# Optimization experiments

Measured on AMD Instinct MI355X. Metric: run time of the kernel, lower is better.

Reference implementation:

```python
import jax, jax.numpy as jnp
import numpy as np

EDGE_DROPOUT = 0.1   # init kwarg edge_dropout
TRAINING = True      # init kwarg is_training
N_NODES = 8192
D_FEAT = 512


def setup_inputs() -> dict:
    key = jax.random.key(0)
    x = jax.random.normal(key, (N_NODES, D_FEAT), dtype=jnp.float32)
    return {"x": x, "k": 30}


def _graph_process(x, k):
    # knn_fast: cosine similarity kNN with symmetric degree normalization.
    n = x.shape[0]
    xn = x / jnp.linalg.norm(x, axis=1, keepdims=True)      # F.normalize(x, dim=1)
    sim = xn @ xn.T                                         # [n, n] (torch does this in blocks of 1000; same math)
    vals, inds = jax.lax.top_k(sim, k + 1)                  # [n, k+1]
    rows = jnp.broadcast_to(jnp.arange(n)[:, None], vals.shape).reshape(-1)
    cols = inds.reshape(-1)
    v = vals.reshape(-1)
    norm_row = vals.sum(axis=1)                             # out-degree mass
    norm_col = jnp.zeros(n, vals.dtype).at[cols].add(v)     # in-degree mass (index_add_)
    norm = norm_row + norm_col
    v = v * (norm[rows] ** -0.5) * (norm[cols] ** -0.5)
    # values[torch.isnan(values)] = 0
    v = jnp.where(jnp.isnan(v), jnp.zeros_like(v), v)
    # symmetrize edge list
    rows_ = jnp.concatenate([rows, cols])
    cols_ = jnp.concatenate([cols, rows])
    v_ = jnp.concatenate([v, v])
    v_ = jax.nn.relu(v_)
    if TRAINING and EDGE_DROPOUT > 0.0:
        keep = jax.random.bernoulli(jax.random.key(42), 1.0 - EDGE_DROPOUT, v_.shape)
        v_ = jnp.where(keep, v_ / (1.0 - EDGE_DROPOUT), jnp.zeros_like(v_))
    # sparse_coo_tensor(...).coalesce(): duplicate (i,j) entries sum -> dense scatter-add
    adj = jnp.zeros((n, n), v_.dtype).at[rows_, cols_].add(v_)
    return adj


def reference(x, k):
    return _graph_process(x, k)
```

## Files before the change

kernel.cpp:

```cpp
#include <hip/hip_runtime.h>
#include <cstdint>
#include <cmath>

#define NN 8192
#define DD 512
#define KP1 31
#define HALF_EDGES (NN * KP1)

typedef float f2 __attribute__((ext_vector_type(2)));

__device__ __forceinline__ uint32_t rotl32(uint32_t v, int s) {
  return (v << s) | (v >> (32 - s));
}

__device__ __forceinline__ void threefry2x32_42(uint32_t x0, uint32_t x1,
                                                uint32_t& o0, uint32_t& o1) {
  const uint32_t ks0 = 0u, ks1 = 42u;
  const uint32_t ks2 = 0x1BD11BDAu ^ ks0 ^ ks1;
  x0 += ks0; x1 += ks1;
  x0 += x1; x1 = rotl32(x1, 13); x1 ^= x0;
  x0 += x1; x1 = rotl32(x1, 15); x1 ^= x0;
  x0 += x1; x1 = rotl32(x1, 26); x1 ^= x0;
  x0 += x1; x1 = rotl32(x1, 6);  x1 ^= x0;
  x0 += ks1; x1 += ks2 + 1u;
  x0 += x1; x1 = rotl32(x1, 17); x1 ^= x0;
  x0 += x1; x1 = rotl32(x1, 29); x1 ^= x0;
  x0 += x1; x1 = rotl32(x1, 16); x1 ^= x0;
  x0 += x1; x1 = rotl32(x1, 24); x1 ^= x0;
  x0 += ks2; x1 += ks0 + 2u;
  x0 += x1; x1 = rotl32(x1, 13); x1 ^= x0;
  x0 += x1; x1 = rotl32(x1, 15); x1 ^= x0;
  x0 += x1; x1 = rotl32(x1, 26); x1 ^= x0;
  x0 += x1; x1 = rotl32(x1, 6);  x1 ^= x0;
  x0 += ks0; x1 += ks1 + 3u;
  x0 += x1; x1 = rotl32(x1, 17); x1 ^= x0;
  x0 += x1; x1 = rotl32(x1, 29); x1 ^= x0;
  x0 += x1; x1 = rotl32(x1, 16); x1 ^= x0;
  x0 += x1; x1 = rotl32(x1, 24); x1 ^= x0;
  x0 += ks1; x1 += ks2 + 4u;
  x0 += x1; x1 = rotl32(x1, 13); x1 ^= x0;
  x0 += x1; x1 = rotl32(x1, 15); x1 ^= x0;
  x0 += x1; x1 = rotl32(x1, 26); x1 ^= x0;
  x0 += x1; x1 = rotl32(x1, 6);  x1 ^= x0;
  x0 += ks2; x1 += ks0 + 5u;
  o0 = x0; o1 = x1;
}

__device__ __forceinline__ bool keep_edge(uint32_t e) {
  uint32_t y0, y1;
  threefry2x32_42(0u, e, y0, y1);
  uint32_t bits = y0 ^ y1;
  float u = __uint_as_float((bits >> 9) | 0x3f800000u) - 1.0f;
  return u < 0.9f;
}

__global__ __launch_bounds__(256) void rownorm_kernel(const float* __restrict__ x,
                                                      float* __restrict__ nrm) {
#pragma clang fp contract(off)
  __shared__ float rowbuf[16][DD];
  __shared__ float partial[16][4];
  int tid = threadIdx.x;
  int rowbase = blockIdx.x * 16;

  for (int p = 0; p < 8; ++p) {
    int f = tid + p * 256;
    int r = f >> 7, k4 = f & 127;
    *(float4*)(&rowbuf[r][k4 << 2]) =
        *(const float4*)(x + (size_t)(rowbase + r) * DD + (k4 << 2));
  }
  __syncthreads();
  if (tid < 64) {
    int r = tid >> 2, q = tid & 3;
    const float* s = &rowbuf[r][q * 128];
    float a0 = s[0]*s[0], a1 = s[1]*s[1], a2 = s[2]*s[2], a3 = s[3]*s[3];
    float a4 = s[4]*s[4], a5 = s[5]*s[5], a6 = s[6]*s[6], a7 = s[7]*s[7];
    for (int i = 8; i < 128; i += 8) {
      a0 += s[i+0]*s[i+0]; a1 += s[i+1]*s[i+1];
      a2 += s[i+2]*s[i+2]; a3 += s[i+3]*s[i+3];
      a4 += s[i+4]*s[i+4]; a5 += s[i+5]*s[i+5];
      a6 += s[i+6]*s[i+6]; a7 += s[i+7]*s[i+7];
    }
    partial[r][q] = ((a0 + a1) + (a2 + a3)) + ((a4 + a5) + (a6 + a7));
  }
  __syncthreads();
  if (tid < 16) {
    float S = (partial[tid][0] + partial[tid][1]) + (partial[tid][2] + partial[tid][3]);
    nrm[rowbase + tid] = sqrtf(S);
  }
}

__global__ __launch_bounds__(256) void xnorm_kernel(const float* __restrict__ x,
                                                    const float* __restrict__ nrm,
                                                    float* __restrict__ xn) {
#pragma clang fp contract(off)
  int idx = blockIdx.x * 256 + threadIdx.x;
  const float4* xv = (const float4*)x;
  float4* xo = (float4*)xn;
  float4 v = xv[idx];
  float n = nrm[idx >> 7];
  v.x = v.x / n; v.y = v.y / n; v.z = v.z / n; v.w = v.w / n;
  xo[idx] = v;
}

template <bool PRE>
__global__ __launch_bounds__(256, 2) void gemm_kernel(const float* __restrict__ x,
                                                      const float* __restrict__ nrm,
                                                      float* __restrict__ out) {
#pragma clang fp contract(off)
  int bid = blockIdx.x;
  int by = (int)((129.0f - sqrtf(16641.0f - 8.0f * (float)bid)) * 0.5f);
  while (64 * by - (by * (by - 1)) / 2 > bid) --by;
  while (64 * (by + 1) - ((by + 1) * by) / 2 <= bid) ++by;
  const int bx = by + (bid - (64 * by - (by * (by - 1)) / 2));

  extern __shared__ char smem[];
  float4* AsF4 = (float4*)smem;
  float*  Bs   = (float*)(smem + 16384);

  const int tid = threadIdx.x;
  const int rb = by * 128;
  const int cb = bx * 128;
  const int m = tid & 7;
  const int g = tid >> 3;

  float nA[4], nB[4];
  if (!PRE) {
    #pragma unroll
    for (int p = 0; p < 4; ++p) {
      nA[p] = nrm[rb + g + 32 * p];
      nB[p] = nrm[cb + g + 32 * p];
    }
  }

  const int lane = tid & 63, wave = tid >> 6;
  const int wr = wave >> 1, wc = wave & 1;
  const int lr = lane >> 3, lc = lane & 7;
  const int r0 = wr * 64 + lr * 8;
  const int c0 = wc * 64 + lc * 8;

  f2 acc[8][4];
  #pragma unroll
  for (int i = 0; i < 8; ++i)
    #pragma unroll
    for (int jp = 0; jp < 4; ++jp) { acc[i][jp].x = 0.f; acc[i][jp].y = 0.f; }

  const float4* xv = (const float4*)x;

  float4 ra[4], rbv[4];
  #pragma unroll
  for (int p = 0; p < 4; ++p) {
    int r = g + 32 * p;
    ra[p]  = xv[(size_t)(rb + r) * 128 + m];
    rbv[p] = xv[(size_t)(cb + r) * 128 + m];
  }

  for (int kc = 0; kc < 16; ++kc) {
    __syncthreads();
    #pragma unroll
    for (int p = 0; p < 4; ++p) {
      int r = g + 32 * p;
      float4 va = ra[p];
      if (!PRE) {
        va.x = va.x / nA[p]; va.y = va.y / nA[p];
        va.z = va.z / nA[p]; va.w = va.w / nA[p];
      }
      AsF4[r * 8 + ((m + (r >> 3)) & 7)] = va;
      float4 vb = rbv[p];
      if (!PRE) {
        vb.x = vb.x / nB[p]; vb.y = vb.y / nB[p];
        vb.z = vb.z / nB[p]; vb.w = vb.w / nB[p];
      }
      float* bp = Bs + (4 * m) * 128 + (r ^ ((m & 3) << 3));
      bp[0]   = vb.x;
      bp[128] = vb.y;
      bp[256] = vb.z;
      bp[384] = vb.w;
    }
    __syncthreads();
    if (kc < 15) {
      #pragma unroll
      for (int p = 0; p < 4; ++p) {
        int r = g + 32 * p;
        ra[p]  = xv[(size_t)(rb + r) * 128 + (kc + 1) * 8 + m];
        rbv[p] = xv[(size_t)(cb + r) * 128 + (kc + 1) * 8 + m];
      }
    }

    #pragma unroll 2
    for (int k4 = 0; k4 < 8; ++k4) {
      float4 av[8];
      const int tA = (k4 + (r0 >> 3)) & 7;
      #pragma unroll
      for (int i = 0; i < 8; ++i) av[i] = AsF4[(r0 + i) * 8 + tA];
      float4 b01[8];
      const int csw = c0 ^ ((k4 & 3) << 3);
      #pragma unroll
      for (int kk = 0; kk < 4; ++kk) {
        const float* bp = Bs + (4 * k4 + kk) * 128 + csw;
        b01[2 * kk]     = *(const float4*)(bp);
        b01[2 * kk + 1] = *(const float4*)(bp + 4);
      }
      #pragma unroll
      for (int kk = 0; kk < 4; ++kk) {
        f2 bb0 = {b01[2 * kk].x,     b01[2 * kk].y};
        f2 bb1 = {b01[2 * kk].z,     b01[2 * kk].w};
        f2 bb2 = {b01[2 * kk + 1].x, b01[2 * kk + 1].y};
        f2 bb3 = {b01[2 * kk + 1].z, b01[2 * kk + 1].w};
        #pragma unroll
        for (int i = 0; i < 8; ++i) {
          float a = ((const float*)&av[i])[kk];
          f2 t0 = a * bb0; acc[i][0] = acc[i][0] + t0;
          f2 t1 = a * bb1; acc[i][1] = acc[i][1] + t1;
          f2 t2 = a * bb2; acc[i][2] = acc[i][2] + t2;
          f2 t3 = a * bb3; acc[i][3] = acc[i][3] + t3;
        }
      }
    }
  }

  float4* outv = (float4*)out;

  #pragma unroll
  for (int i = 0; i < 8; ++i) {
    #pragma unroll
    for (int h = 0; h < 2; ++h) {
      float4 o;
      o.x = acc[i][2 * h].x;     o.y = acc[i][2 * h].y;
      o.z = acc[i][2 * h + 1].x; o.w = acc[i][2 * h + 1].y;
      outv[(size_t)(rb + r0 + i) * 2048 + ((cb + c0) >> 2) + h] = o;
    }
  }

  if (rb != cb) {
    float* Cs = (float*)smem;
    #pragma unroll 1
    for (int q = 0; q < 4; ++q) {
      __syncthreads();
      if (wr == (q >> 1) && (lr >> 2) == (q & 1)) {
        const int rB = (lr & 3) * 8;
        #pragma unroll
        for (int i = 0; i < 8; ++i) {
          #pragma unroll
          for (int jp = 0; jp < 4; ++jp)
            *(f2*)(Cs + (rB + i) * 130 + wc * 64 + lc * 8 + 2 * jp) = acc[i][jp];
        }
      }
      __syncthreads();
      #pragma unroll
      for (int q2 = 0; q2 < 4; ++q2) {
        int f = tid + q2 * 256;
        int c = f >> 3, t4 = f & 7;
        float4 o;
        o.x = Cs[(4 * t4 + 0) * 130 + c];
        o.y = Cs[(4 * t4 + 1) * 130 + c];
        o.z = Cs[(4 * t4 + 2) * 130 + c];
        o.w = Cs[(4 * t4 + 3) * 130 + c];
        outv[(size_t)(cb + c) * 2048 + ((rb + q * 32) >> 2) + t4] = o;
      }
    }
  }
}

__global__ __launch_bounds__(256) void topk_kernel(const float* __restrict__ sim,
                                                   float* __restrict__ vals,
                                                   int* __restrict__ inds) {
  const int w = threadIdx.x >> 6;
  const int lane = threadIdx.x & 63;
  const int row = blockIdx.x * 4 + w;

  float kval = -1e30f;
  int   kidx = 0;
  float kmin = -1e30f;

  const float* srow = sim + (size_t)row * NN;
  for (int grp = 0; grp < NN / 64; ++grp) {
    float v = srow[grp * 64 + lane];
    unsigned long long mask = __ballot(v > kmin);
    while (mask) {
      int src = __builtin_ctzll(mask);
      mask &= mask - 1;
      float vv = __shfl(v, src, 64);
      if (vv > kmin) {
        int cc = grp * 64 + src;
        unsigned long long ge = __ballot(kval >= vv) & 0x7FFFFFFFull;
        int pos = __popcll(ge);
        float upv = __shfl_up(kval, 1, 64);
        int   upi = __shfl_up(kidx, 1, 64);
        if (lane < KP1) {
          if (lane == pos) { kval = vv; kidx = cc; }
          else if (lane > pos) { kval = upv; kidx = upi; }
        }
        kmin = __shfl(kval, KP1 - 1, 64);
      }
    }
  }
  if (lane < KP1) {
    vals[(size_t)row * KP1 + lane] = kval;
    inds[row * KP1 + lane] = kidx;
  }
}

__global__ __launch_bounds__(256) void norm_kernel(const float* __restrict__ vals,
                                                   const int* __restrict__ inds,
                                                   float* __restrict__ norm) {
  int i = blockIdx.x * blockDim.x + threadIdx.x;
  if (i >= NN) return;
  float s = 0.f;
  for (int t = 0; t < KP1; ++t) {
    float v = vals[i * KP1 + t];
    s += v;
    atomicAdd(&norm[inds[i * KP1 + t]], v);
  }
  atomicAdd(&norm[i], s);
}

__global__ __launch_bounds__(256) void scatter_kernel(const float* __restrict__ vals,
                                                      const int* __restrict__ inds,
                                                      const float* __restrict__ norm,
                                                      float* __restrict__ out) {
  int e = blockIdx.x * blockDim.x + threadIdx.x;
  if (e >= HALF_EDGES) return;
  int i = e / KP1;
  int c = inds[e];
  float v = vals[e];
  float nv = v * (1.0f / sqrtf(norm[i])) * (1.0f / sqrtf(norm[c]));
  if (isnan(nv)) nv = 0.f;
  nv = fmaxf(nv, 0.f);
  float scaled = nv / 0.9f;
  if (keep_edge((uint32_t)e))
    atomicAdd(out + (size_t)i * NN + c, scaled);
  if (keep_edge((uint32_t)(e + HALF_EDGES)))
    atomicAdd(out + (size_t)c * NN + i, scaled);
}

extern "C" void kernel_launch(void* const* d_in, const int* in_sizes, int n_in,
                              void* d_out, int out_size, void* d_ws, size_t ws_size,
                              hipStream_t stream) {
  (void)in_sizes; (void)n_in;
  const float* x = (const float*)d_in[0];
  float* out = (float*)d_out;

  float* nrm  = (float*)d_ws;
  float* vals = nrm + NN;
  int*   inds = (int*)(vals + HALF_EDGES);
  float* norm = (float*)(inds + HALF_EDGES);
  float* xn   = (float*)((char*)d_ws + (size_t)(2 * 1024 * 1024));
  const bool pre = ws_size >= (size_t)(2 * 1024 * 1024) + (size_t)NN * DD * 4;

  hipLaunchKernelGGL(rownorm_kernel, dim3(NN / 16), dim3(256), 0, stream, x, nrm);
  if (pre) {
    hipLaunchKernelGGL(xnorm_kernel, dim3(NN * DD / 4 / 256), dim3(256), 0, stream,
                       x, nrm, xn);
    hipLaunchKernelGGL((gemm_kernel<true>), dim3(2080), dim3(256), 32768, stream,
                       xn, (const float*)nullptr, out);
  } else {
    hipLaunchKernelGGL((gemm_kernel<false>), dim3(2080), dim3(256), 32768, stream,
                       x, nrm, out);
  }
  hipLaunchKernelGGL(topk_kernel, dim3(NN / 4), dim3(256), 0, stream,
                     out, vals, inds);
  hipMemsetAsync(norm, 0, NN * sizeof(float), stream);
  hipLaunchKernelGGL(norm_kernel, dim3((NN + 255) / 256), dim3(256), 0, stream,
                     vals, inds, norm);
  hipMemsetAsync(d_out, 0, (size_t)out_size * sizeof(float), stream);
  hipLaunchKernelGGL(scatter_kernel, dim3((HALF_EDGES + 255) / 256), dim3(256), 0, stream,
                     vals, inds, norm, out);
}
```

Measured before the change: 1.103 ms.

## Double-buffer GEMM tiles and stage A via direct global-to-LDS loads

Replaces the templated GEMM with a dedicated pre-normalized kernel that uses K-chunks of 16 with double-buffered shared memory. The A tile is loaded with global_load_lds, which writes straight into LDS without passing through registers, while the B tile is prefetched two stages ahead through registers. This needs one barrier per iteration instead of two, overlapping loads with FMA work and cutting register pressure. The fallback path keeps the old design under a new name. The risks are more loop iterations and correctness of the swizzle and async-load ordering.

Measured after the change: 1.111 ms. Within noise of the previous version (+0.8%).

```diff
diff --git a/kernel.cpp b/kernel.cpp
--- a/kernel.cpp
+++ b/kernel.cpp
@@ -54,6 +54,12 @@
   return u < 0.9f;
 }
 
+__device__ __forceinline__ void gll16(const float4* gsrc, void* lds) {
+  __builtin_amdgcn_global_load_lds(
+      (const __attribute__((address_space(1))) uint32_t*)gsrc,
+      (__attribute__((address_space(3))) uint32_t*)lds, 16, 0, 0);
+}
+
 __global__ __launch_bounds__(256) void rownorm_kernel(const float* __restrict__ x,
                                                       float* __restrict__ nrm) {
 #pragma clang fp contract(off)
@@ -102,10 +108,8 @@
   xo[idx] = v;
 }
 
-template <bool PRE>
-__global__ __launch_bounds__(256, 2) void gemm_kernel(const float* __restrict__ x,
-                                                      const float* __restrict__ nrm,
-                                                      float* __restrict__ out) {
+__global__ __launch_bounds__(256, 2) void gemm_kernel_pre(const float* __restrict__ x,
+                                                          float* __restrict__ out) {
 #pragma clang fp contract(off)
   int bid = blockIdx.x;
   int by = (int)((129.0f - sqrtf(16641.0f - 8.0f * (float)bid)) * 0.5f);
@@ -113,6 +117,164 @@
   while (64 * (by + 1) - ((by + 1) * by) / 2 <= bid) ++by;
   const int bx = by + (bid - (64 * by - (by * (by - 1)) / 2));
 
+  __shared__ __align__(16) char smem[32768];
+  float4* AsF4 = (float4*)smem;
+  float*  Bs   = (float*)(smem + 16384);
+
+  const int tid = threadIdx.x;
+  const int rb = by * 128;
+  const int cb = bx * 128;
+  const int m = tid & 3;
+  const int g = tid >> 2;
+
+  const int lane = tid & 63, wave = tid >> 6;
+  const int wr = wave >> 1, wc = wave & 1;
+  const int lr = lane >> 3, lc = lane & 7;
+  const int r0 = wr * 64 + lr * 8;
+  const int c0 = wc * 64 + lc * 8;
+  const int r3 = r0 >> 3;
+
+  f2 acc[8][4];
+  #pragma unroll
+  for (int i = 0; i < 8; ++i)
+    #pragma unroll
+    for (int jp = 0; jp < 4; ++jp) { acc[i][jp].x = 0.f; acc[i][jp].y = 0.f; }
+
+  const float4* xv = (const float4*)x;
+  float4 rbv[2];
+
+  int gr[2], gs[2];
+  #pragma unroll
+  for (int q = 0; q < 2; ++q) {
+    int fi = wave * 128 + q * 64 + lane;
+    gr[q] = fi >> 2;
+    gs[q] = ((fi & 3) - (gr[q] >> 3)) & 3;
+  }
+
+  auto stage_A = [&](int nbuf, int t) {
+    #pragma unroll
+    for (int q = 0; q < 2; ++q)
+      gll16(xv + (size_t)(rb + gr[q]) * 128 + t * 4 + gs[q],
+            (void*)(AsF4 + nbuf * 512 + wave * 128 + q * 64));
+  };
+  auto load_B = [&](int t) {
+    #pragma unroll
+    for (int p = 0; p < 2; ++p)
+      rbv[p] = xv[(size_t)(cb + g + 64 * p) * 128 + t * 4 + m];
+  };
+  auto write_B = [&](int nbuf) {
+    #pragma unroll
+    for (int p = 0; p < 2; ++p) {
+      int r = g + 64 * p;
+      float* bp = Bs + nbuf * 2048 + (4 * m) * 128 + (r ^ (m << 3));
+      bp[0]   = rbv[p].x;
+      bp[128] = rbv[p].y;
+      bp[256] = rbv[p].z;
+      bp[384] = rbv[p].w;
+    }
+  };
+
+  load_B(0);
+  write_B(0);
+  stage_A(0, 0);
+  load_B(1);
+
+  #pragma unroll 1
+  for (int t = 0; t < 32; ++t) {
+    const int buf = t & 1;
+    __syncthreads();
+    if (t < 31) {
+      stage_A(buf ^ 1, t + 1);
+      write_B(buf ^ 1);
+      if (t < 30) load_B(t + 2);
+    }
+    const float4* Ab = AsF4 + buf * 512;
+    const float*  Bb = Bs + buf * 2048;
+    #pragma unroll
+    for (int k4 = 0; k4 < 4; ++k4) {
+      float4 av[8];
+      const int tA = (k4 + r3) & 3;
+      #pragma unroll
+      for (int i = 0; i < 8; ++i) av[i] = Ab[(r0 + i) * 4 + tA];
+      const int csw = c0 ^ (k4 << 3);
+      #pragma unroll
+      for (int kk = 0; kk < 4; ++kk) {
+        const float* bp = Bb + (4 * k4 + kk) * 128 + csw;
+        float4 b0 = *(const float4*)(bp);
+        float4 b1 = *(const float4*)(bp + 4);
+        f2 bb0 = {b0.x, b0.y};
+        f2 bb1 = {b0.z, b0.w};
+        f2 bb2 = {b1.x, b1.y};
+        f2 bb3 = {b1.z, b1.w};
+        #pragma unroll
+        for (int i = 0; i < 8; ++i) {
+          float a = ((const float*)&av[i])[kk];
+          f2 t0 = a * bb0;
+          f2 t1 = a * bb1;
+          f2 t2 = a * bb2;
+          f2 t3 = a * bb3;
+          acc[i][0] = acc[i][0] + t0;
+          acc[i][1] = acc[i][1] + t1;
+          acc[i][2] = acc[i][2] + t2;
+          acc[i][3] = acc[i][3] + t3;
+        }
+      }
+    }
+  }
+
+  float4* outv = (float4*)out;
+
+  #pragma unroll
+  for (int i = 0; i < 8; ++i) {
+    #pragma unroll
+    for (int h = 0; h < 2; ++h) {
+      float4 o;
+      o.x = acc[i][2 * h].x;     o.y = acc[i][2 * h].y;
+      o.z = acc[i][2 * h + 1].x; o.w = acc[i][2 * h + 1].y;
+      outv[(size_t)(rb + r0 + i) * 2048 + ((cb + c0) >> 2) + h] = o;
+    }
+  }
+
+  if (rb != cb) {
+    float* Cs = (float*)smem;
+    #pragma unroll 1
+    for (int q = 0; q < 4; ++q) {
+      __syncthreads();
+      if (wr == (q >> 1) && (lr >> 2) == (q & 1)) {
+        const int rB = (lr & 3) * 8;
+        #pragma unroll
+        for (int i = 0; i < 8; ++i) {
+          #pragma unroll
+          for (int jp = 0; jp < 4; ++jp)
+            *(f2*)(Cs + (rB + i) * 130 + wc * 64 + lc * 8 + 2 * jp) = acc[i][jp];
+        }
+      }
+      __syncthreads();
+      #pragma unroll
+      for (int q2 = 0; q2 < 4; ++q2) {
+        int f = tid + q2 * 256;
+        int c = f >> 3, t4 = f & 7;
+        float4 o;
+        o.x = Cs[(4 * t4 + 0) * 130 + c];
+        o.y = Cs[(4 * t4 + 1) * 130 + c];
+        o.z = Cs[(4 * t4 + 2) * 130 + c];
+        o.w = Cs[(4 * t4 + 3) * 130 + c];
+        outv[(size_t)(cb + c) * 2048 + ((rb + q * 32) >> 2) + t4] = o;
+      }
+    }
+  }
+}
+
+__global__ __launch_bounds__(256, 2) void gemm_kernel_fb(const float* __restrict__ x,
+                                                         const float* __restrict__ nrm,
+                                                         float* __restrict__ out) {
+#pragma clang fp contract(off)
+  int bid = blockIdx.x;
+  int by = (int)((129.0f - sqrtf(16641.0f - 8.0f * (float)bid)) * 0.5f);
+  while (64 * by - (by * (by - 1)) / 2 > bid) --by;
+  while (64 * (by + 1) - ((by + 1) * by) / 2 <= bid) ++by;
+  const int bx = by + (bid - (64 * by - (by * (by - 1)) / 2));
+
   extern __shared__ char smem[];
   float4* AsF4 = (float4*)smem;
   float*  Bs   = (float*)(smem + 16384);
@@ -124,12 +286,10 @@
   const int g = tid >> 3;
 
   float nA[4], nB[4];
-  if (!PRE) {
-    #pragma unroll
-    for (int p = 0; p < 4; ++p) {
-      nA[p] = nrm[rb + g + 32 * p];
-      nB[p] = nrm[cb + g + 32 * p];
-    }
+  #pragma unroll
+  for (int p = 0; p < 4; ++p) {
+    nA[p] = nrm[rb + g + 32 * p];
+    nB[p] = nrm[cb + g + 32 * p];
   }
 
   const int lane = tid & 63, wave = tid >> 6;
@@ -137,6 +297,7 @@
   const int lr = lane >> 3, lc = lane & 7;
   const int r0 = wr * 64 + lr * 8;
   const int c0 = wc * 64 + lc * 8;
+  const int r3 = r0 >> 3;
 
   f2 acc[8][4];
   #pragma unroll
@@ -145,7 +306,6 @@
     for (int jp = 0; jp < 4; ++jp) { acc[i][jp].x = 0.f; acc[i][jp].y = 0.f; }
 
   const float4* xv = (const float4*)x;
-
   float4 ra[4], rbv[4];
   #pragma unroll
   for (int p = 0; p < 4; ++p) {
@@ -160,17 +320,13 @@
     for (int p = 0; p < 4; ++p) {
       int r = g + 32 * p;
       float4 va = ra[p];
-      if (!PRE) {
-        va.x = va.x / nA[p]; va.y = va.y / nA[p];
-        va.z = va.z / nA[p]; va.w = va.w / nA[p];
-      }
+      va.x = va.x / nA[p]; va.y = va.y / nA[p];
+      va.z = va.z / nA[p]; va.w = va.w / nA[p];
       AsF4[r * 8 + ((m + (r >> 3)) & 7)] = va;
       float4 vb = rbv[p];
-      if (!PRE) {
-        vb.x = vb.x / nB[p]; vb.y = vb.y / nB[p];
-        vb.z = vb.z / nB[p]; vb.w = vb.w / nB[p];
-      }
-      float* bp = Bs + (4 * m) * 128 + (r ^ ((m & 3) << 3));
+      vb.x = vb.x / nB[p]; vb.y = vb.y / nB[p];
+      vb.z = vb.z / nB[p]; vb.w = vb.w / nB[p];
+      float* bp = Bs + (4 * m) * 128 + (r ^ (m << 3));
       bp[0]   = vb.x;
       bp[128] = vb.y;
       bp[256] = vb.z;
@@ -189,11 +345,11 @@
     #pragma unroll 2
     for (int k4 = 0; k4 < 8; ++k4) {
       float4 av[8];
-      const int tA = (k4 + (r0 >> 3)) & 7;
+      const int tA = (k4 + r3) & 7;
       #pragma unroll
       for (int i = 0; i < 8; ++i) av[i] = AsF4[(r0 + i) * 8 + tA];
       float4 b01[8];
-      const int csw = c0 ^ ((k4 & 3) << 3);
+      const int csw = c0 ^ (k4 << 3);
       #pragma unroll
       for (int kk = 0; kk < 4; ++kk) {
         const float* bp = Bs + (4 * k4 + kk) * 128 + csw;
@@ -209,17 +365,20 @@
         #pragma unroll
         for (int i = 0; i < 8; ++i) {
           float a = ((const float*)&av[i])[kk];
-          f2 t0 = a * bb0; acc[i][0] = acc[i][0] + t0;
-          f2 t1 = a * bb1; acc[i][1] = acc[i][1] + t1;
-          f2 t2 = a * bb2; acc[i][2] = acc[i][2] + t2;
-          f2 t3 = a * bb3; acc[i][3] = acc[i][3] + t3;
+          f2 t0 = a * bb0;
+          f2 t1 = a * bb1;
+          f2 t2 = a * bb2;
+          f2 t3 = a * bb3;
+          acc[i][0] = acc[i][0] + t0;
+          acc[i][1] = acc[i][1] + t1;
+          acc[i][2] = acc[i][2] + t2;
+          acc[i][3] = acc[i][3] + t3;
         }
       }
     }
   }
 
   float4* outv = (float4*)out;
-
   #pragma unroll
   for (int i = 0; i < 8; ++i) {
     #pragma unroll
@@ -230,7 +389,6 @@
       outv[(size_t)(rb + r0 + i) * 2048 + ((cb + c0) >> 2) + h] = o;
     }
   }
-
   if (rb != cb) {
     float* Cs = (float*)smem;
     #pragma unroll 1
@@ -351,10 +509,10 @@
   if (pre) {
     hipLaunchKernelGGL(xnorm_kernel, dim3(NN * DD / 4 / 256), dim3(256), 0, stream,
                        x, nrm, xn);
-    hipLaunchKernelGGL((gemm_kernel<true>), dim3(2080), dim3(256), 32768, stream,
-                       xn, (const float*)nullptr, out);
+    hipLaunchKernelGGL(gemm_kernel_pre, dim3(2080), dim3(256), 0, stream,
+                       xn, out);
   } else {
-    hipLaunchKernelGGL((gemm_kernel<false>), dim3(2080), dim3(256), 32768, stream,
+    hipLaunchKernelGGL(gemm_kernel_fb, dim3(2080), dim3(256), 32768, stream,
                        x, nrm, out);
   }
   hipLaunchKernelGGL(topk_kernel, dim3(NN / 4), dim3(256), 0, stream,
```

## Fuse norm with transpose and use 1024-thread async-LDS GEMM with swizzled tile order

Applied to the files above, without the earlier changes.

Merges the row-norm and normalize kernels into one kernel that also writes the normalized matrix transposed (k-major), so the GEMM can stage contiguous tiles straight into LDS with global_load_lds in a double-buffered loop. The new GEMM runs 1024 threads per block with a 4x4 register tile, remaps block ids to interleave triangle tiles, and writes the mirrored tile directly with transposed stores instead of going through LDS. It drops one pass over x and the register-staged loads. In exchange each thread keeps a much smaller register tile, which lowers arithmetic intensity per LDS read, and the transposed writes of the mirror tile are strided. The fallback GEMM also gets a tweaked B-swizzle.

Result: slower. 1.150 ms (+4.3%).

```diff
diff --git a/kernel.cpp b/kernel.cpp
--- a/kernel.cpp
+++ b/kernel.cpp
@@ -54,6 +54,12 @@
   return u < 0.9f;
 }
 
+__device__ __forceinline__ void gll16(const float4* gsrc, void* lds) {
+  __builtin_amdgcn_global_load_lds(
+      (const __attribute__((address_space(1))) uint32_t*)gsrc,
+      (__attribute__((address_space(3))) uint32_t*)lds, 16, 0, 0);
+}
+
 __global__ __launch_bounds__(256) void rownorm_kernel(const float* __restrict__ x,
                                                       float* __restrict__ nrm) {
 #pragma clang fp contract(off)
@@ -89,23 +95,154 @@
   }
 }
 
-__global__ __launch_bounds__(256) void xnorm_kernel(const float* __restrict__ x,
-                                                    const float* __restrict__ nrm,
-                                                    float* __restrict__ xn) {
+__global__ __launch_bounds__(256) void normT_kernel(const float* __restrict__ x,
+                                                    float* __restrict__ nrm,
+                                                    float* __restrict__ xnt) {
 #pragma clang fp contract(off)
-  int idx = blockIdx.x * 256 + threadIdx.x;
-  const float4* xv = (const float4*)x;
-  float4* xo = (float4*)xn;
-  float4 v = xv[idx];
-  float n = nrm[idx >> 7];
-  v.x = v.x / n; v.y = v.y / n; v.z = v.z / n; v.w = v.w / n;
-  xo[idx] = v;
-}
-
-template <bool PRE>
-__global__ __launch_bounds__(256, 2) void gemm_kernel(const float* __restrict__ x,
-                                                      const float* __restrict__ nrm,
-                                                      float* __restrict__ out) {
+  __shared__ float rowbuf[16][DD];
+  __shared__ float partial[16][4];
+  __shared__ float snrm[16];
+  int tid = threadIdx.x;
+  int rowbase = blockIdx.x * 16;
+
+  for (int p = 0; p < 8; ++p) {
+    int f = tid + p * 256;
+    int r = f >> 7, k4 = f & 127;
+    *(float4*)(&rowbuf[r][k4 << 2]) =
+        *(const float4*)(x + (size_t)(rowbase + r) * DD + (k4 << 2));
+  }
+  __syncthreads();
+  if (tid < 64) {
+    int r = tid >> 2, q = tid & 3;
+    const float* s = &rowbuf[r][q * 128];
+    float a0 = s[0]*s[0], a1 = s[1]*s[1], a2 = s[2]*s[2], a3 = s[3]*s[3];
+    float a4 = s[4]*s[4], a5 = s[5]*s[5], a6 = s[6]*s[6], a7 = s[7]*s[7];
+    for (int i = 8; i < 128; i += 8) {
+      a0 += s[i+0]*s[i+0]; a1 += s[i+1]*s[i+1];
+      a2 += s[i+2]*s[i+2]; a3 += s[i+3]*s[i+3];
+      a4 += s[i+4]*s[i+4]; a5 += s[i+5]*s[i+5];
+      a6 += s[i+6]*s[i+6]; a7 += s[i+7]*s[i+7];
+    }
+    partial[r][q] = ((a0 + a1) + (a2 + a3)) + ((a4 + a5) + (a6 + a7));
+  }
+  __syncthreads();
+  if (tid < 16) {
+    float S = (partial[tid][0] + partial[tid][1]) + (partial[tid][2] + partial[tid][3]);
+    float n = sqrtf(S);
+    nrm[rowbase + tid] = n;
+    snrm[tid] = n;
+  }
+  __syncthreads();
+  for (int kq = 0; kq < 2; ++kq) {
+    int k = tid * 2 + kq;
+    #pragma unroll
+    for (int rq = 0; rq < 4; ++rq) {
+      float4 o;
+      o.x = rowbuf[rq * 4 + 0][k] / snrm[rq * 4 + 0];
+      o.y = rowbuf[rq * 4 + 1][k] / snrm[rq * 4 + 1];
+      o.z = rowbuf[rq * 4 + 2][k] / snrm[rq * 4 + 2];
+      o.w = rowbuf[rq * 4 + 3][k] / snrm[rq * 4 + 3];
+      *(float4*)(xnt + (size_t)k * NN + rowbase + rq * 4) = o;
+    }
+  }
+}
+
+__global__ __launch_bounds__(1024) void gemm_kernel_pre2(const float* __restrict__ xnt,
+                                                         float* __restrict__ out) {
+#pragma clang fp contract(off)
+  int bid0 = blockIdx.x;
+  int bid = (bid0 & 7) * 260 + (bid0 >> 3);
+  int by = (int)((129.0f - sqrtf(16641.0f - 8.0f * (float)bid)) * 0.5f);
+  while (64 * by - (by * (by - 1)) / 2 > bid) --by;
+  while (64 * (by + 1) - ((by + 1) * by) / 2 <= bid) ++by;
+  const int bx = by + (bid - (64 * by - (by * (by - 1)) / 2));
+
+  __shared__ __align__(16) char smem[32768];
+  float* As = (float*)smem;
+  float* Bs = (float*)(smem + 16384);
+
+  const int tid  = threadIdx.x;
+  const int lane = tid & 63, wave = tid >> 6;
+  const int rb = by * 128, cb = bx * 128;
+
+  const int wr = wave >> 2, wc = wave & 3;
+  const int lr = lane >> 3, lc = lane & 7;
+  const int r0 = wr * 32 + lr * 4;
+  const int c0 = wc * 32 + lc * 4;
+
+  f2 acc[4][2];
+  #pragma unroll
+  for (int i = 0; i < 4; ++i) {
+    acc[i][0].x = 0.f; acc[i][0].y = 0.f;
+    acc[i][1].x = 0.f; acc[i][1].y = 0.f;
+  }
+
+  const bool stA = wave < 8;
+  const int w8 = stA ? wave : wave - 8;
+  const int kl = w8 * 2 + (lane >> 5);
+  const size_t gcol = (size_t)(stA ? rb : cb) + (lane & 31) * 4;
+  float* ldst = (stA ? As : Bs) + w8 * 256;
+
+  auto stage = [&](int nbuf, int t) {
+    gll16((const float4*)(xnt + (size_t)(t * 16 + kl) * NN + gcol),
+          (void*)(ldst + nbuf * 2048));
+  };
+
+  stage(0, 0);
+
+  #pragma unroll 1
+  for (int t = 0; t < 32; ++t) {
+    const int buf = t & 1;
+    __syncthreads();
+    if (t < 31) stage(buf ^ 1, t + 1);
+    const float* Ab = As + buf * 2048 + r0;
+    const float* Bb = Bs + buf * 2048 + c0;
+    #pragma unroll
+    for (int k = 0; k < 16; ++k) {
+      float4 a = *(const float4*)(Ab + k * 128);
+      float4 b = *(const float4*)(Bb + k * 128);
+      f2 bb0 = {b.x, b.y};
+      f2 bb1 = {b.z, b.w};
+      #pragma unroll
+      for (int i = 0; i < 4; ++i) {
+        float av = ((const float*)&a)[i];
+        f2 t0 = av * bb0;
+        f2 t1 = av * bb1;
+        acc[i][0] = acc[i][0] + t0;
+        acc[i][1] = acc[i][1] + t1;
+      }
+    }
+  }
+
+  float4* outv = (float4*)out;
+
+  #pragma unroll
+  for (int i = 0; i < 4; ++i) {
+    float4 o;
+    o.x = acc[i][0].x; o.y = acc[i][0].y;
+    o.z = acc[i][1].x; o.w = acc[i][1].y;
+    outv[(size_t)(rb + r0 + i) * 2048 + ((cb + c0) >> 2)] = o;
+  }
+  if (rb != cb) {
+    #pragma unroll
+    for (int j = 0; j < 4; ++j) {
+      const int jh = j >> 1;
+      float4 o;
+      if (j & 1) {
+        o.x = acc[0][jh].y; o.y = acc[1][jh].y;
+        o.z = acc[2][jh].y; o.w = acc[3][jh].y;
+      } else {
+        o.x = acc[0][jh].x; o.y = acc[1][jh].x;
+        o.z = acc[2][jh].x; o.w = acc[3][jh].x;
+      }
+      outv[(size_t)(cb + c0 + j) * 2048 + ((rb + r0) >> 2)] = o;
+    }
+  }
+}
+
+__global__ __launch_bounds__(256, 2) void gemm_kernel_fb(const float* __restrict__ x,
+                                                         const float* __restrict__ nrm,
+                                                         float* __restrict__ out) {
 #pragma clang fp contract(off)
   int bid = blockIdx.x;
   int by = (int)((129.0f - sqrtf(16641.0f - 8.0f * (float)bid)) * 0.5f);
@@ -124,12 +261,10 @@
   const int g = tid >> 3;
 
   float nA[4], nB[4];
-  if (!PRE) {
-    #pragma unroll
-    for (int p = 0; p < 4; ++p) {
-      nA[p] = nrm[rb + g + 32 * p];
-      nB[p] = nrm[cb + g + 32 * p];
-    }
+  #pragma unroll
+  for (int p = 0; p < 4; ++p) {
+    nA[p] = nrm[rb + g + 32 * p];
+    nB[p] = nrm[cb + g + 32 * p];
   }
 
   const int lane = tid & 63, wave = tid >> 6;
@@ -137,6 +272,7 @@
   const int lr = lane >> 3, lc = lane & 7;
   const int r0 = wr * 64 + lr * 8;
   const int c0 = wc * 64 + lc * 8;
+  const int r3 = r0 >> 3;
 
   f2 acc[8][4];
   #pragma unroll
@@ -145,7 +281,6 @@
     for (int jp = 0; jp < 4; ++jp) { acc[i][jp].x = 0.f; acc[i][jp].y = 0.f; }
 
   const float4* xv = (const float4*)x;
-
   float4 ra[4], rbv[4];
   #pragma unroll
   for (int p = 0; p < 4; ++p) {
@@ -160,17 +295,13 @@
     for (int p = 0; p < 4; ++p) {
       int r = g + 32 * p;
       float4 va = ra[p];
-      if (!PRE) {
-        va.x = va.x / nA[p]; va.y = va.y / nA[p];
-        va.z = va.z / nA[p]; va.w = va.w / nA[p];
-      }
+      va.x = va.x / nA[p]; va.y = va.y / nA[p];
+      va.z = va.z / nA[p]; va.w = va.w / nA[p];
       AsF4[r * 8 + ((m + (r >> 3)) & 7)] = va;
       float4 vb = rbv[p];
-      if (!PRE) {
-        vb.x = vb.x / nB[p]; vb.y = vb.y / nB[p];
-        vb.z = vb.z / nB[p]; vb.w = vb.w / nB[p];
-      }
-      float* bp = Bs + (4 * m) * 128 + (r ^ ((m & 3) << 3));
+      vb.x = vb.x / nB[p]; vb.y = vb.y / nB[p];
+      vb.z = vb.z / nB[p]; vb.w = vb.w / nB[p];
+      float* bp = Bs + (4 * m) * 128 + (r ^ (m << 3));
       bp[0]   = vb.x;
       bp[128] = vb.y;
       bp[256] = vb.z;
@@ -189,11 +320,11 @@
     #pragma unroll 2
     for (int k4 = 0; k4 < 8; ++k4) {
       float4 av[8];
-      const int tA = (k4 + (r0 >> 3)) & 7;
+      const int tA = (k4 + r3) & 7;
       #pragma unroll
       for (int i = 0; i < 8; ++i) av[i] = AsF4[(r0 + i) * 8 + tA];
       float4 b01[8];
-      const int csw = c0 ^ ((k4 & 3) << 3);
+      const int csw = c0 ^ (k4 << 3);
       #pragma unroll
       for (int kk = 0; kk < 4; ++kk) {
         const float* bp = Bs + (4 * k4 + kk) * 128 + csw;
@@ -209,17 +340,20 @@
         #pragma unroll
         for (int i = 0; i < 8; ++i) {
           float a = ((const float*)&av[i])[kk];
-          f2 t0 = a * bb0; acc[i][0] = acc[i][0] + t0;
-          f2 t1 = a * bb1; acc[i][1] = acc[i][1] + t1;
-          f2 t2 = a * bb2; acc[i][2] = acc[i][2] + t2;
-          f2 t3 = a * bb3; acc[i][3] = acc[i][3] + t3;
+          f2 t0 = a * bb0;
+          f2 t1 = a * bb1;
+          f2 t2 = a * bb2;
+          f2 t3 = a * bb3;
+          acc[i][0] = acc[i][0] + t0;
+          acc[i][1] = acc[i][1] + t1;
+          acc[i][2] = acc[i][2] + t2;
+          acc[i][3] = acc[i][3] + t3;
         }
       }
     }
   }
 
   float4* outv = (float4*)out;
-
   #pragma unroll
   for (int i = 0; i < 8; ++i) {
     #pragma unroll
@@ -230,7 +364,6 @@
       outv[(size_t)(rb + r0 + i) * 2048 + ((cb + c0) >> 2) + h] = o;
     }
   }
-
   if (rb != cb) {
     float* Cs = (float*)smem;
     #pragma unroll 1
@@ -344,17 +477,17 @@
   float* vals = nrm + NN;
   int*   inds = (int*)(vals + HALF_EDGES);
   float* norm = (float*)(inds + HALF_EDGES);
-  float* xn   = (float*)((char*)d_ws + (size_t)(2 * 1024 * 1024));
-  const bool pre = ws_size >= (size_t)(2 * 1024 * 1024) + (size_t)NN * DD * 4;
-
-  hipLaunchKernelGGL(rownorm_kernel, dim3(NN / 16), dim3(256), 0, stream, x, nrm);
-  if (pre) {
-    hipLaunchKernelGGL(xnorm_kernel, dim3(NN * DD / 4 / 256), dim3(256), 0, stream,
-                       x, nrm, xn);
-    hipLaunchKernelGGL((gemm_kernel<true>), dim3(2080), dim3(256), 32768, stream,
-                       xn, (const float*)nullptr, out);
+  float* xnt  = (float*)((char*)d_ws + (size_t)(2 * 1024 * 1024));
+  const bool pre2 = ws_size >= (size_t)(2 * 1024 * 1024) + (size_t)NN * DD * 4;
+
+  if (pre2) {
+    hipLaunchKernelGGL(normT_kernel, dim3(NN / 16), dim3(256), 0, stream,
+                       x, nrm, xnt);
+    hipLaunchKernelGGL(gemm_kernel_pre2, dim3(2080), dim3(1024), 0, stream,
+                       xnt, out);
   } else {
-    hipLaunchKernelGGL((gemm_kernel<false>), dim3(2080), dim3(256), 32768, stream,
+    hipLaunchKernelGGL(rownorm_kernel, dim3(NN / 16), dim3(256), 0, stream, x, nrm);
+    hipLaunchKernelGGL(gemm_kernel_fb, dim3(2080), dim3(256), 32768, stream,
                        x, nrm, out);
   }
   hipLaunchKernelGGL(topk_kernel, dim3(NN / 4), dim3(256), 0, stream,
```
